# Optimization experiments

Hardware: AMD Instinct MI355X
Metric: run time of the kernel (lower is better)

Reference implementation:

```python
import jax, jax.numpy as jnp
import numpy as np

EMBED = 32
HEADS = 8
HEAD_DIM = EMBED // HEADS  # 4


def setup_inputs() -> dict:
    key = jax.random.key(0)
    ks = jax.random.split(key, 12)
    N, Q, K = 4, 2048, 2048
    inp = {
        "query": jax.random.normal(ks[0], (N, Q, EMBED), dtype=jnp.float32),
        "key": jax.random.normal(ks[1], (N, K, EMBED), dtype=jnp.float32),
        "value": jax.random.normal(ks[2], (N, K, EMBED), dtype=jnp.float32),
        "mask": jnp.ones((N, 1, Q, K), dtype=jnp.int32),
        # nn.Linear params: W stored as (in, out) here; math y = x @ W + b
        "Wq": jax.random.normal(ks[3], (EMBED, EMBED), dtype=jnp.float32) / np.sqrt(EMBED),
        "bq": jax.random.normal(ks[4], (EMBED,), dtype=jnp.float32) * 0.01,
        "Wk": jax.random.normal(ks[5], (EMBED, EMBED), dtype=jnp.float32) / np.sqrt(EMBED),
        "bk": jax.random.normal(ks[6], (EMBED,), dtype=jnp.float32) * 0.01,
        "Wv": jax.random.normal(ks[7], (EMBED, EMBED), dtype=jnp.float32) / np.sqrt(EMBED),
        "bv": jax.random.normal(ks[8], (EMBED,), dtype=jnp.float32) * 0.01,
        "Wo": jax.random.normal(ks[9], (EMBED, EMBED), dtype=jnp.float32) / np.sqrt(EMBED),
        "bo": jax.random.normal(ks[10], (EMBED,), dtype=jnp.float32) * 0.01,
    }
    return inp


def reference(query, key, value, mask, Wq, bq, Wk, bk, Wv, bv, Wo, bo):
    N, Qlen, _ = query.shape
    Klen = key.shape[1]
    # linear projections
    q = (query @ Wq + bq).reshape(N, Qlen, HEADS, HEAD_DIM)
    k = (key @ Wk + bk).reshape(N, Klen, HEADS, HEAD_DIM)
    v = (value @ Wv + bv).reshape(N, Klen, HEADS, HEAD_DIM)
    # energy: [N, H, Q, K]
    energy = jnp.einsum("nqhd,nkhd->nhqk", q, k)
    energy = jnp.where(mask == 0, jnp.float32(-1e20), energy)
    # NOTE: original scales by sqrt(embedSize), not sqrt(headDim)
    attn = jax.nn.softmax(energy / jnp.sqrt(jnp.float32(EMBED)), axis=3)
    out = jnp.einsum("nhqv,nvhd->nqhd", attn, v).reshape(N, Qlen, EMBED)
    return out @ Wo + bo
```

## Files before the change

### kernel.cpp

```cpp
#include <hip/hip_runtime.h>

#define NB 4
#define SEQ 2048
#define EMB 32
#define HEADS 8
#define HD 4

typedef float v2f __attribute__((ext_vector_type(2)));

__device__ __forceinline__ v2f splat2(float x) { v2f r; r.x = x; r.y = x; return r; }
__device__ __forceinline__ v2f pkfma(v2f a, v2f b, v2f c) {
  return __builtin_elementwise_fma(a, b, c);
}

__global__ __launch_bounds__(256) void proj_kv_kernel(
    const float* __restrict__ key, const float* __restrict__ value,
    const float* __restrict__ Wk, const float* __restrict__ bk,
    const float* __restrict__ Wv, const float* __restrict__ bv,
    float* __restrict__ Kp, float* __restrict__ Vp) {
  const int half = NB * SEQ / 8;
  bool isV = blockIdx.x >= half;
  const float* X = isV ? value : key;
  const float* W = isV ? Wv : Wk;
  const float* b = isV ? bv : bk;
  float* P = isV ? Vp : Kp;
  int blk = isV ? (blockIdx.x - half) : blockIdx.x;

  __shared__ float sW[EMB][EMB];
  __shared__ float sb[EMB];
  __shared__ float sX[8][EMB];
  int t = threadIdx.x;
  for (int i = t; i < EMB * EMB; i += 256) sW[i >> 5][i & 31] = W[i];
  if (t < EMB) sb[t] = b[t];
  size_t row0 = (size_t)blk * 8;
  int r = t >> 5, c = t & 31;
  sX[r][c] = X[(row0 + r) * EMB + c];
  __syncthreads();
  float acc = sb[c];
#pragma unroll
  for (int d = 0; d < EMB; ++d) acc = fmaf(sX[r][d], sW[d][c], acc);
  P[(row0 + r) * EMB + c] = acc;
}

__device__ __forceinline__ void load_tile(
    const float*& kptr, const float*& vptr,
    const int*& mp0, const int*& mp1, const int*& mp2, const int*& mp3,
    float4 (&KK)[4], float4 (&VV)[4], int4 (&MQ)[4]) {
  KK[0] = *(const float4*)(kptr);
  KK[1] = *(const float4*)(kptr + EMB);
  KK[2] = *(const float4*)(kptr + 2 * EMB);
  KK[3] = *(const float4*)(kptr + 3 * EMB);
  VV[0] = *(const float4*)(vptr);
  VV[1] = *(const float4*)(vptr + EMB);
  VV[2] = *(const float4*)(vptr + 2 * EMB);
  VV[3] = *(const float4*)(vptr + 3 * EMB);
  MQ[0] = *(const int4*)(mp0);
  MQ[1] = *(const int4*)(mp1);
  MQ[2] = *(const int4*)(mp2);
  MQ[3] = *(const int4*)(mp3);
  kptr += 32 * EMB; vptr += 32 * EMB;
  mp0 += 32; mp1 += 32; mp2 += 32; mp3 += 32;
}

__device__ __forceinline__ void compute_tile(
    const float4 (&KK)[4], const float4 (&VV)[4], const int4 (&MQ)[4],
    const v2f (&q2)[2][4], v2f (&l2)[2], v2f (&ac2)[2][4]) {
#pragma unroll
  for (int p = 0; p < 2; ++p) {
    const int4 mA = MQ[2 * p], mB = MQ[2 * p + 1];
    v2f psum = splat2(0.0f);
#pragma unroll
    for (int j = 0; j < 4; ++j) {
      const float4 kk = KK[j];
      v2f s = pkfma(q2[p][0], splat2(kk.x),
              pkfma(q2[p][1], splat2(kk.y),
              pkfma(q2[p][2], splat2(kk.z), q2[p][3] * splat2(kk.w))));
      int ma_ = (j == 0) ? mA.x : (j == 1) ? mA.y : (j == 2) ? mA.z : mA.w;
      int mb_ = (j == 0) ? mB.x : (j == 1) ? mB.y : (j == 2) ? mB.z : mB.w;
      v2f pp;
      pp.x = ma_ ? __builtin_amdgcn_exp2f(s.x) : 0.0f;
      pp.y = mb_ ? __builtin_amdgcn_exp2f(s.y) : 0.0f;
      psum += pp;
      const float4 vv = VV[j];
      ac2[p][0] = pkfma(pp, splat2(vv.x), ac2[p][0]);
      ac2[p][1] = pkfma(pp, splat2(vv.y), ac2[p][1]);
      ac2[p][2] = pkfma(pp, splat2(vv.z), ac2[p][2]);
      ac2[p][3] = pkfma(pp, splat2(vv.w), ac2[p][3]);
    }
    l2[p] += psum;
  }
}

__global__ __launch_bounds__(256, 2) void attn_kernel(
    const float* __restrict__ query, const int* __restrict__ mask,
    const float* __restrict__ Kp, const float* __restrict__ Vp,
    const float* __restrict__ Wq, const float* __restrict__ bq,
    const float* __restrict__ Wo, const float* __restrict__ bo,
    float* __restrict__ out) {
  __shared__ float sWq[EMB][EMB];
  __shared__ float sWo[EMB][EMB];
  __shared__ float sbq[EMB];
  __shared__ float sbo[EMB];
  __shared__ float sX[16][EMB];
  __shared__ float sCtx[16][EMB + 1];

  int t = threadIdx.x;
  int n = blockIdx.x >> 7;
  int qt = blockIdx.x & 127;
  int qrow0 = qt * 16;

  int rl = t >> 6;
  int lane = t & 63;
  int h = lane & 7;
  int ks = lane >> 3;

  for (int i = t; i < EMB * EMB; i += 256) {
    sWq[i >> 5][i & 31] = Wq[i];
    sWo[i >> 5][i & 31] = Wo[i];
  }
  if (t < EMB) { sbq[t] = bq[t]; sbo[t] = bo[t]; }
  {
    int r = t >> 5, c = t & 31;
    sX[r][c] = query[((size_t)n * SEQ + qrow0 + r) * EMB + c];
    sX[r + 8][c] = query[((size_t)n * SEQ + qrow0 + r + 8) * EMB + c];
  }
  __syncthreads();

  const float SC = 0.17677669529663687f * 1.4426950408889634f;
  float q[4][4];
#pragma unroll
  for (int r = 0; r < 4; ++r)
#pragma unroll
    for (int d = 0; d < 4; ++d) q[r][d] = sbq[4 * h + d];
#pragma unroll
  for (int j = 0; j < EMB; ++j) {
    float w0 = sWq[j][4 * h + 0], w1 = sWq[j][4 * h + 1];
    float w2 = sWq[j][4 * h + 2], w3 = sWq[j][4 * h + 3];
#pragma unroll
    for (int r = 0; r < 4; ++r) {
      float x = sX[4 * rl + r][j];
      q[r][0] = fmaf(x, w0, q[r][0]);
      q[r][1] = fmaf(x, w1, q[r][1]);
      q[r][2] = fmaf(x, w2, q[r][2]);
      q[r][3] = fmaf(x, w3, q[r][3]);
    }
  }
  v2f q2[2][4];
#pragma unroll
  for (int p = 0; p < 2; ++p)
#pragma unroll
    for (int d = 0; d < 4; ++d) {
      q2[p][d].x = q[2 * p][d] * SC;
      q2[p][d].y = q[2 * p + 1][d] * SC;
    }

  const float* kptr = Kp + (size_t)n * SEQ * EMB + (size_t)(4 * ks) * EMB + 4 * h;
  const float* vptr = Vp + (size_t)n * SEQ * EMB + (size_t)(4 * ks) * EMB + 4 * h;
  size_t rb = (size_t)n * SEQ + qrow0 + 4 * rl;
  const int* mp0 = mask + (rb + 0) * SEQ + 4 * ks;
  const int* mp1 = mask + (rb + 1) * SEQ + 4 * ks;
  const int* mp2 = mask + (rb + 2) * SEQ + 4 * ks;
  const int* mp3 = mask + (rb + 3) * SEQ + 4 * ks;

  v2f l2[2], ac2[2][4];
#pragma unroll
  for (int p = 0; p < 2; ++p) {
    l2[p] = splat2(0.0f);
#pragma unroll
    for (int d = 0; d < 4; ++d) ac2[p][d] = splat2(0.0f);
  }

  float4 ka[4], va[4]; int4 ma[4];
  float4 kb[4], vb[4]; int4 mb[4];
  load_tile(kptr, vptr, mp0, mp1, mp2, mp3, ka, va, ma);
  for (int i = 0; i < 31; ++i) {
    load_tile(kptr, vptr, mp0, mp1, mp2, mp3, kb, vb, mb);
    compute_tile(ka, va, ma, q2, l2, ac2);
    load_tile(kptr, vptr, mp0, mp1, mp2, mp3, ka, va, ma);
    compute_tile(kb, vb, mb, q2, l2, ac2);
  }
  load_tile(kptr, vptr, mp0, mp1, mp2, mp3, kb, vb, mb);
  compute_tile(ka, va, ma, q2, l2, ac2);
  compute_tile(kb, vb, mb, q2, l2, ac2);

#pragma unroll
  for (int d = 8; d <= 32; d <<= 1) {
#pragma unroll
    for (int p = 0; p < 2; ++p) {
      l2[p].x += __shfl_xor(l2[p].x, d);
      l2[p].y += __shfl_xor(l2[p].y, d);
#pragma unroll
      for (int e = 0; e < 4; ++e) {
        ac2[p][e].x += __shfl_xor(ac2[p][e].x, d);
        ac2[p][e].y += __shfl_xor(ac2[p][e].y, d);
      }
    }
  }

  if (ks < 4) {
#pragma unroll
    for (int p = 0; p < 2; ++p) {
      float invA = __builtin_amdgcn_rcpf(l2[p].x);
      float invB = __builtin_amdgcn_rcpf(l2[p].y);
      float vA = (ks == 0) ? ac2[p][0].x : (ks == 1) ? ac2[p][1].x
               : (ks == 2) ? ac2[p][2].x : ac2[p][3].x;
      float vB = (ks == 0) ? ac2[p][0].y : (ks == 1) ? ac2[p][1].y
               : (ks == 2) ? ac2[p][2].y : ac2[p][3].y;
      sCtx[4 * rl + 2 * p + 0][4 * h + ks] = vA * invA;
      sCtx[4 * rl + 2 * p + 1][4 * h + ks] = vB * invB;
    }
  }
  __syncthreads();

  int e = t & 31;
#pragma unroll
  for (int rr = 0; rr < 2; ++rr) {
    int r = (t >> 5) + 8 * rr;
    float o = sbo[e];
#pragma unroll
    for (int j = 0; j < EMB; ++j) o = fmaf(sCtx[r][j], sWo[j][e], o);
    out[((size_t)n * SEQ + qrow0 + r) * EMB + e] = o;
  }
}

extern "C" void kernel_launch(void* const* d_in, const int* in_sizes, int n_in,
                              void* d_out, int out_size, void* d_ws, size_t ws_size,
                              hipStream_t stream) {
  const float* query = (const float*)d_in[0];
  const float* key   = (const float*)d_in[1];
  const float* value = (const float*)d_in[2];
  const int*   mask  = (const int*)d_in[3];
  const float* Wq = (const float*)d_in[4];
  const float* bq = (const float*)d_in[5];
  const float* Wk = (const float*)d_in[6];
  const float* bk = (const float*)d_in[7];
  const float* Wv = (const float*)d_in[8];
  const float* bv = (const float*)d_in[9];
  const float* Wo = (const float*)d_in[10];
  const float* bo = (const float*)d_in[11];
  float* out = (float*)d_out;

  float* Kp = (float*)d_ws;
  float* Vp = Kp + (size_t)NB * SEQ * EMB;

  proj_kv_kernel<<<dim3(2 * NB * SEQ / 8), dim3(256), 0, stream>>>(
      key, value, Wk, bk, Wv, bv, Kp, Vp);
  attn_kernel<<<dim3(NB * (SEQ / 16)), dim3(256), 0, stream>>>(
      query, mask, Kp, Vp, Wq, bq, Wo, bo, out);
}
```

Baseline: 67.57 us.

## Pre-pack int32 mask into bitmasks and add an all-ones fast path

Adds a separate kernel that packs the int32 attention mask into 32-bit words, one bit per key, so the attention kernel loads four words per tile instead of four int4 vectors. The attention loop now always computes the exponentials, then zeroes masked entries only when a tile is not fully unmasked, which removes the per-element selects from the common path and reduces register and load pressure. In exchange, the full 64MB mask is still read once, now in an extra standalone bandwidth-bound launch that can no longer overlap with the attention arithmetic.

```diff
diff --git a/kernel.cpp b/kernel.cpp
--- a/kernel.cpp
+++ b/kernel.cpp
@@ -7,10 +7,25 @@
 #define HD 4
 
 typedef float v2f __attribute__((ext_vector_type(2)));
+typedef unsigned int uint;
 
 __device__ __forceinline__ v2f splat2(float x) { v2f r; r.x = x; r.y = x; return r; }
 __device__ __forceinline__ v2f pkfma(v2f a, v2f b, v2f c) {
   return __builtin_elementwise_fma(a, b, c);
+}
+
+__global__ __launch_bounds__(256) void mask_pack_kernel(
+    const int* __restrict__ mask, uint* __restrict__ pmw) {
+  int g = blockIdx.x * 256 + threadIdx.x;
+  const int4 v = ((const int4*)mask)[g];
+  uint nib = (uint)(v.x != 0) | ((uint)(v.y != 0) << 1) |
+             ((uint)(v.z != 0) << 2) | ((uint)(v.w != 0) << 3);
+  int lane = threadIdx.x & 63;
+  uint w = nib << (4 * (lane & 7));
+  w |= __shfl_xor(w, 1);
+  w |= __shfl_xor(w, 2);
+  w |= __shfl_xor(w, 4);
+  if ((lane & 7) == 0) pmw[g >> 3] = w;
 }
 
 __global__ __launch_bounds__(256) void proj_kv_kernel(
@@ -43,9 +58,8 @@
 }
 
 __device__ __forceinline__ void load_tile(
-    const float*& kptr, const float*& vptr,
-    const int*& mp0, const int*& mp1, const int*& mp2, const int*& mp3,
-    float4 (&KK)[4], float4 (&VV)[4], int4 (&MQ)[4]) {
+    const float*& kptr, const float*& vptr, const uint*& mwp,
+    float4 (&KK)[4], float4 (&VV)[4], uint4& MW) {
   KK[0] = *(const float4*)(kptr);
   KK[1] = *(const float4*)(kptr + EMB);
   KK[2] = *(const float4*)(kptr + 2 * EMB);
@@ -54,45 +68,55 @@
   VV[1] = *(const float4*)(vptr + EMB);
   VV[2] = *(const float4*)(vptr + 2 * EMB);
   VV[3] = *(const float4*)(vptr + 3 * EMB);
-  MQ[0] = *(const int4*)(mp0);
-  MQ[1] = *(const int4*)(mp1);
-  MQ[2] = *(const int4*)(mp2);
-  MQ[3] = *(const int4*)(mp3);
-  kptr += 32 * EMB; vptr += 32 * EMB;
-  mp0 += 32; mp1 += 32; mp2 += 32; mp3 += 32;
+  MW.x = mwp[0];
+  MW.y = mwp[64];
+  MW.z = mwp[128];
+  MW.w = mwp[192];
+  kptr += 32 * EMB; vptr += 32 * EMB; mwp += 1;
 }
 
 __device__ __forceinline__ void compute_tile(
-    const float4 (&KK)[4], const float4 (&VV)[4], const int4 (&MQ)[4],
+    const float4 (&KK)[4], const float4 (&VV)[4], const uint4& MW, int ks4,
     const v2f (&q2)[2][4], v2f (&l2)[2], v2f (&ac2)[2][4]) {
+  v2f pf[2][4];
 #pragma unroll
   for (int p = 0; p < 2; ++p) {
-    const int4 mA = MQ[2 * p], mB = MQ[2 * p + 1];
-    v2f psum = splat2(0.0f);
 #pragma unroll
     for (int j = 0; j < 4; ++j) {
       const float4 kk = KK[j];
       v2f s = pkfma(q2[p][0], splat2(kk.x),
               pkfma(q2[p][1], splat2(kk.y),
               pkfma(q2[p][2], splat2(kk.z), q2[p][3] * splat2(kk.w))));
-      int ma_ = (j == 0) ? mA.x : (j == 1) ? mA.y : (j == 2) ? mA.z : mA.w;
-      int mb_ = (j == 0) ? mB.x : (j == 1) ? mB.y : (j == 2) ? mB.z : mB.w;
-      v2f pp;
-      pp.x = ma_ ? __builtin_amdgcn_exp2f(s.x) : 0.0f;
-      pp.y = mb_ ? __builtin_amdgcn_exp2f(s.y) : 0.0f;
-      psum += pp;
+      pf[p][j].x = __builtin_amdgcn_exp2f(s.x);
+      pf[p][j].y = __builtin_amdgcn_exp2f(s.y);
+    }
+  }
+  uint allm = MW.x & MW.y & MW.z & MW.w;
+  if (allm != 0xFFFFFFFFu) {
+#pragma unroll
+    for (int j = 0; j < 4; ++j) {
+      if (!((MW.x >> (ks4 + j)) & 1u)) pf[0][j].x = 0.0f;
+      if (!((MW.y >> (ks4 + j)) & 1u)) pf[0][j].y = 0.0f;
+      if (!((MW.z >> (ks4 + j)) & 1u)) pf[1][j].x = 0.0f;
+      if (!((MW.w >> (ks4 + j)) & 1u)) pf[1][j].y = 0.0f;
+    }
+  }
+#pragma unroll
+  for (int p = 0; p < 2; ++p) {
+    l2[p] += (pf[p][0] + pf[p][1]) + (pf[p][2] + pf[p][3]);
+#pragma unroll
+    for (int j = 0; j < 4; ++j) {
       const float4 vv = VV[j];
-      ac2[p][0] = pkfma(pp, splat2(vv.x), ac2[p][0]);
-      ac2[p][1] = pkfma(pp, splat2(vv.y), ac2[p][1]);
-      ac2[p][2] = pkfma(pp, splat2(vv.z), ac2[p][2]);
-      ac2[p][3] = pkfma(pp, splat2(vv.w), ac2[p][3]);
-    }
-    l2[p] += psum;
+      ac2[p][0] = pkfma(pf[p][j], splat2(vv.x), ac2[p][0]);
+      ac2[p][1] = pkfma(pf[p][j], splat2(vv.y), ac2[p][1]);
+      ac2[p][2] = pkfma(pf[p][j], splat2(vv.z), ac2[p][2]);
+      ac2[p][3] = pkfma(pf[p][j], splat2(vv.w), ac2[p][3]);
+    }
   }
 }
 
 __global__ __launch_bounds__(256, 2) void attn_kernel(
-    const float* __restrict__ query, const int* __restrict__ mask,
+    const float* __restrict__ query, const uint* __restrict__ pmw,
     const float* __restrict__ Kp, const float* __restrict__ Vp,
     const float* __restrict__ Wq, const float* __restrict__ bq,
     const float* __restrict__ Wo, const float* __restrict__ bo,
@@ -113,6 +137,7 @@
   int lane = t & 63;
   int h = lane & 7;
   int ks = lane >> 3;
+  int ks4 = 4 * ks;
 
   for (int i = t; i < EMB * EMB; i += 256) {
     sWq[i >> 5][i & 31] = Wq[i];
@@ -154,13 +179,10 @@
       q2[p][d].y = q[2 * p + 1][d] * SC;
     }
 
-  const float* kptr = Kp + (size_t)n * SEQ * EMB + (size_t)(4 * ks) * EMB + 4 * h;
-  const float* vptr = Vp + (size_t)n * SEQ * EMB + (size_t)(4 * ks) * EMB + 4 * h;
+  const float* kptr = Kp + (size_t)n * SEQ * EMB + (size_t)ks4 * EMB + 4 * h;
+  const float* vptr = Vp + (size_t)n * SEQ * EMB + (size_t)ks4 * EMB + 4 * h;
   size_t rb = (size_t)n * SEQ + qrow0 + 4 * rl;
-  const int* mp0 = mask + (rb + 0) * SEQ + 4 * ks;
-  const int* mp1 = mask + (rb + 1) * SEQ + 4 * ks;
-  const int* mp2 = mask + (rb + 2) * SEQ + 4 * ks;
-  const int* mp3 = mask + (rb + 3) * SEQ + 4 * ks;
+  const uint* mwp = pmw + rb * (SEQ / 32);
 
   v2f l2[2], ac2[2][4];
 #pragma unroll
@@ -170,18 +192,18 @@
     for (int d = 0; d < 4; ++d) ac2[p][d] = splat2(0.0f);
   }
 
-  float4 ka[4], va[4]; int4 ma[4];
-  float4 kb[4], vb[4]; int4 mb[4];
-  load_tile(kptr, vptr, mp0, mp1, mp2, mp3, ka, va, ma);
+  float4 ka[4], va[4]; uint4 ma;
+  float4 kb[4], vb[4]; uint4 mb;
+  load_tile(kptr, vptr, mwp, ka, va, ma);
   for (int i = 0; i < 31; ++i) {
-    load_tile(kptr, vptr, mp0, mp1, mp2, mp3, kb, vb, mb);
-    compute_tile(ka, va, ma, q2, l2, ac2);
-    load_tile(kptr, vptr, mp0, mp1, mp2, mp3, ka, va, ma);
-    compute_tile(kb, vb, mb, q2, l2, ac2);
-  }
-  load_tile(kptr, vptr, mp0, mp1, mp2, mp3, kb, vb, mb);
-  compute_tile(ka, va, ma, q2, l2, ac2);
-  compute_tile(kb, vb, mb, q2, l2, ac2);
+    load_tile(kptr, vptr, mwp, kb, vb, mb);
+    compute_tile(ka, va, ma, ks4, q2, l2, ac2);
+    load_tile(kptr, vptr, mwp, ka, va, ma);
+    compute_tile(kb, vb, mb, ks4, q2, l2, ac2);
+  }
+  load_tile(kptr, vptr, mwp, kb, vb, mb);
+  compute_tile(ka, va, ma, ks4, q2, l2, ac2);
+  compute_tile(kb, vb, mb, ks4, q2, l2, ac2);
 
 #pragma unroll
   for (int d = 8; d <= 32; d <<= 1) {
@@ -242,9 +264,12 @@
 
   float* Kp = (float*)d_ws;
   float* Vp = Kp + (size_t)NB * SEQ * EMB;
-
+  uint* pmw = (uint*)(Vp + (size_t)NB * SEQ * EMB);
+
+  mask_pack_kernel<<<dim3(NB * SEQ * SEQ / 4 / 256), dim3(256), 0, stream>>>(
+      mask, pmw);
   proj_kv_kernel<<<dim3(2 * NB * SEQ / 8), dim3(256), 0, stream>>>(
       key, value, Wk, bk, Wv, bv, Kp, Vp);
   attn_kernel<<<dim3(NB * (SEQ / 16)), dim3(256), 0, stream>>>(
-      query, mask, Kp, Vp, Wq, bq, Wo, bo, out);
-}
+      query, pmw, Kp, Vp, Wq, bq, Wo, bo, out);
+}
```

Result: no change. 67.87 us (+0.4%).
